# Performance work log

Hardware: AMD Instinct MI355X
Metric: run time of the kernel (lower is better)

The kernel has to match this reference:

```python
import jax, jax.numpy as jnp
import numpy as np

B, T, H, A, V, L = 4096, 16, 768, 128, 16, 2

def setup_inputs() -> dict:
    key = jax.random.key(0)
    ks = jax.random.split(key, 8)
    s = 0.02
    return {
        "last_hidden": jax.random.normal(ks[0], (B, T, H), jnp.float32),
        "attention_mask": jnp.ones((B, T), jnp.int64),
        "variety_ids": jax.random.randint(ks[1], (B,), 0, V),
        "Wd": jax.random.normal(ks[2], (V, H, A), jnp.float32) * s,  # per-variety down-proj
        "bd": jnp.zeros((V, A), jnp.float32),
        "Wu": jax.random.normal(ks[3], (V, A, H), jnp.float32) * s,  # per-variety up-proj
        "bu": jnp.zeros((V, H), jnp.float32),
        "Wc": jax.random.normal(ks[4], (L, H), jnp.float32) * s,     # classifier
        "bc": jnp.zeros((L,), jnp.float32),
    }

def reference(last_hidden, attention_mask, variety_ids, Wd, bd, Wu, bu, Wc, bc):
    x = last_hidden[:, 0, :]                                   # (B,H) CLS token
    # Dense grouped adapter: run all V bottleneck adapters, then select per example.
    h = jax.nn.gelu(jnp.einsum('bh,vha->bva', x, Wd) + bd[None])   # (B,V,A)
    u = jnp.einsum('bva,vah->bvh', h, Wu) + bu[None]               # (B,V,H)
    sel = u[jnp.arange(x.shape[0]), variety_ids]                   # (B,H) routed output
    adapted = x + sel                                              # residual bottleneck adapter
    # dropout is identity at p=0.0 / eval
    return adapted @ Wc.T + bc                                     # (B,L) logits
```

## Files before the change

### kernel.cpp

```cpp
#include <hip/hip_runtime.h>
#include <hip/hip_bf16.h>

#define BB 4096
#define TT 16
#define HH 768
#define AA 128
#define VV 16
#define LL 2
#define NCHUNK 6
#define MT 64

typedef __attribute__((ext_vector_type(8))) short short8v;
typedef __attribute__((ext_vector_type(4))) float float4v;

#define WS_OFFS 0
#define WS_ROWS 64
#define WS_WUC  4160
#define WS_BUC  8256
#define WS_WDP  8448

__device__ __forceinline__ unsigned short f2bf(float f) {
    __hip_bfloat16 h = __float2bfloat16(f);
    return *reinterpret_cast<unsigned short*>(&h);
}

__device__ __forceinline__ float gelu_tanh(float z) {
    float y = 0.7978845608028654f * (z + 0.044715f * z * z * z);
    y = fminf(fmaxf(y, -15.f), 15.f);
    float e = __expf(2.f * y);
    float th = (e - 1.f) / (e + 1.f);
    return 0.5f * z * (1.f + th);
}

__global__ __launch_bounds__(256) void k_prep(
    const int*   __restrict__ variety_ids,
    const float* __restrict__ Wd,
    const float* __restrict__ Wu,
    const float* __restrict__ bu,
    const float* __restrict__ Wc,
    int* __restrict__ ws_i)
{
    __shared__ __align__(16) unsigned short Wds[128 * 136];
    __shared__ float sp0[256], sp1[256];
    __shared__ int hist[VV], hoff[VV + 1], hcur[VV];

    const int t = threadIdx.x;
    const int bid = blockIdx.x;
    unsigned short* wdp = (unsigned short*)(ws_i + WS_WDP);
    float* Wuc = (float*)(ws_i + WS_WUC);
    float* buc = (float*)(ws_i + WS_BUC);

    if (bid < 96) {
        const int v = bid / NCHUNK, kc = bid % NCHUNK;
        const float* wd = Wd + (size_t)v * HH * AA;
        const int ks0 = kc * 128;
        #pragma unroll
        for (int s = 0; s < 16; ++s) {
            int idx = t + s * 256;
            int hl  = idx >> 5;
            int a4  = idx & 31;
            float4 wv = *(const float4*)(wd + (size_t)(ks0 + hl) * AA + a4 * 4);
            Wds[(a4 * 4 + 0) * 136 + hl] = f2bf(wv.x);
            Wds[(a4 * 4 + 1) * 136 + hl] = f2bf(wv.y);
            Wds[(a4 * 4 + 2) * 136 + hl] = f2bf(wv.z);
            Wds[(a4 * 4 + 3) * 136 + hl] = f2bf(wv.w);
        }
        __syncthreads();
        unsigned short* dst = wdp + (size_t)(v * NCHUNK + kc) * AA * 128;
        #pragma unroll
        for (int s = 0; s < 8; ++s) {
            int G = t + s * 256;
            int a = G >> 4, g = G & 15;
            uint4 w = *(const uint4*)&Wds[a * 136 + g * 8];
            *(uint4*)&dst[a * 128 + g * 8] = w;
        }
    } else if (bid < 128) {
        const int v  = (bid - 96) >> 1;
        const int ah = (bid - 96) & 1;
        const int a  = ah * 64 + (t >> 2);
        const int q  = t & 3;
        const float* wu = Wu + (size_t)v * AA * HH + (size_t)a * HH;
        float s0 = 0.f, s1 = 0.f;
        #pragma unroll 4
        for (int h = q * 192; h < q * 192 + 192; h += 4) {
            float4 w  = *(const float4*)&wu[h];
            float4 c0 = *(const float4*)&Wc[h];
            float4 c1 = *(const float4*)&Wc[HH + h];
            s0 += w.x * c0.x + w.y * c0.y + w.z * c0.z + w.w * c0.w;
            s1 += w.x * c1.x + w.y * c1.y + w.z * c1.z + w.w * c1.w;
        }
        sp0[t] = s0; sp1[t] = s1;
        __syncthreads();
        if (t < 64) {
            float r0 = sp0[t * 4] + sp0[t * 4 + 1] + sp0[t * 4 + 2] + sp0[t * 4 + 3];
            float r1 = sp1[t * 4] + sp1[t * 4 + 1] + sp1[t * 4 + 2] + sp1[t * 4 + 3];
            int aa = ah * 64 + t;
            Wuc[(v * AA + aa) * LL + 0] = r0;
            Wuc[(v * AA + aa) * LL + 1] = r1;
        }
    } else if (bid == 128) {
        const int pair = t >> 3, seg = t & 7;
        const int v = pair >> 1, l = pair & 1;
        float s = 0.f;
        const float* bv = bu + (size_t)v * HH;
        for (int h = seg * 96; h < seg * 96 + 96; ++h) s += bv[h] * Wc[l * HH + h];
        sp0[t] = s;
        __syncthreads();
        if (t < 32) {
            float r = 0.f;
            #pragma unroll
            for (int i = 0; i < 8; ++i) r += sp0[t * 8 + i];
            buc[t] = r;
        }
    } else {
        if (t < VV) hist[t] = 0;
        __syncthreads();
        for (int b = t; b < BB; b += 256) atomicAdd(&hist[variety_ids[b]], 1);
        __syncthreads();
        if (t == 0) {
            int s = 0;
            for (int i = 0; i < VV; ++i) { hoff[i] = s; s += hist[i]; }
            hoff[VV] = s;
            for (int i = 0; i <= VV; ++i) ws_i[WS_OFFS + i] = hoff[i];
        }
        __syncthreads();
        if (t < VV) hcur[t] = hoff[t];
        __syncthreads();
        for (int b = t; b < BB; b += 256) {
            int v = variety_ids[b];
            int p = atomicAdd(&hcur[v], 1);
            ws_i[WS_ROWS + p] = b;
        }
    }
}

__global__ __launch_bounds__(256) void k_main(
    const float* __restrict__ last_hidden,
    const int*   __restrict__ ws_i,
    const float* __restrict__ bd,
    const float* __restrict__ Wc,
    const float* __restrict__ bc,
    float* __restrict__ out)
{
    __shared__ __align__(16) unsigned short Xs[MT * 136];
    __shared__ __align__(16) unsigned short Wds[128 * 136];
    __shared__ __align__(16) unsigned short WcB[16 * 136];
    __shared__ int srows[MT];
    __shared__ float xc[MT * LL];

    const int* offs = ws_i + WS_OFFS;
    const int* rows = ws_i + WS_ROWS;
    const float* Wuc = (const float*)(ws_i + WS_WUC);
    const float* buc = (const float*)(ws_i + WS_BUC);
    const unsigned short* wdp = (const unsigned short*)(ws_i + WS_WDP);
    const int t = threadIdx.x;

    const int rt = blockIdx.x;
    int v = -1, tloc = 0, cnt = 0, obase = 0, acc_t = 0;
    for (int vv = 0; vv < VV; ++vv) {
        int c  = offs[vv + 1] - offs[vv];
        int nt = (c + MT - 1) / MT;
        if (rt < acc_t + nt) {
            v = vv; tloc = rt - acc_t;
            cnt = c - tloc * MT; if (cnt > MT) cnt = MT;
            obase = offs[vv];
            break;
        }
        acc_t += nt;
    }
    if (v < 0) return;

    if (t < MT) {
        int rr = t < cnt ? t : cnt - 1;
        srows[t] = rows[obase + tloc * MT + rr];
    }

    const int lane = t & 63;
    const int wv_  = t >> 6;
    const int wr = (wv_ >> 1) * 32;
    const int wc = (wv_ & 1) * 64;
    const int m = lane & 15, quad = lane >> 4;

    float4v acc[2][4];
    float4v accx[2];
    #pragma unroll
    for (int i = 0; i < 2; ++i) {
        accx[i] = (float4v){0.f, 0.f, 0.f, 0.f};
        #pragma unroll
        for (int j = 0; j < 4; ++j)
            acc[i][j] = (float4v){0.f, 0.f, 0.f, 0.f};
    }

    for (int kc = 0; kc < NCHUNK; ++kc) {
        const int ks0 = kc * 128;
        __syncthreads();
        #pragma unroll
        for (int s = 0; s < 8; ++s) {
            int idx = t + s * 256;
            int r   = idx >> 5;
            int k4  = idx & 31;
            const float* xr = last_hidden + (size_t)srows[r] * TT * HH + ks0 + k4 * 4;
            float4 xv = *(const float4*)xr;
            unsigned int p0 = (unsigned)f2bf(xv.x) | ((unsigned)f2bf(xv.y) << 16);
            unsigned int p1 = (unsigned)f2bf(xv.z) | ((unsigned)f2bf(xv.w) << 16);
            *(uint2*)&Xs[r * 136 + k4 * 4] = make_uint2(p0, p1);
        }
        {
            const unsigned short* wb = wdp + (size_t)(v * NCHUNK + kc) * AA * 128;
            #pragma unroll
            for (int s = 0; s < 8; ++s) {
                int G = t + s * 256;
                int a = G >> 4, g = G & 15;
                uint4 w = *(const uint4*)&wb[a * 128 + g * 8];
                *(uint4*)&Wds[a * 136 + g * 8] = w;
            }
        }
        {
            int c = t >> 4, g = t & 15;
            uint4 w = make_uint4(0u, 0u, 0u, 0u);
            if (c < LL) {
                const float* wcr = Wc + (size_t)c * HH + ks0 + g * 8;
                float4 w0 = *(const float4*)wcr;
                float4 w1 = *(const float4*)(wcr + 4);
                w.x = (unsigned)f2bf(w0.x) | ((unsigned)f2bf(w0.y) << 16);
                w.y = (unsigned)f2bf(w0.z) | ((unsigned)f2bf(w0.w) << 16);
                w.z = (unsigned)f2bf(w1.x) | ((unsigned)f2bf(w1.y) << 16);
                w.w = (unsigned)f2bf(w1.z) | ((unsigned)f2bf(w1.w) << 16);
            }
            *(uint4*)&WcB[c * 136 + g * 8] = w;
        }
        __syncthreads();

        #pragma unroll
        for (int k0 = 0; k0 < 128; k0 += 32) {
            short8v af[2], bf[4];
            #pragma unroll
            for (int i = 0; i < 2; ++i)
                af[i] = *(const short8v*)&Xs[(wr + i * 16 + m) * 136 + k0 + quad * 8];
            #pragma unroll
            for (int j = 0; j < 4; ++j)
                bf[j] = *(const short8v*)&Wds[(wc + j * 16 + m) * 136 + k0 + quad * 8];
            #pragma unroll
            for (int i = 0; i < 2; ++i)
                #pragma unroll
                for (int j = 0; j < 4; ++j)
                    acc[i][j] = __builtin_amdgcn_mfma_f32_16x16x32_bf16(af[i], bf[j], acc[i][j], 0, 0, 0);
            if (wc == 0) {
                short8v cf = *(const short8v*)&WcB[m * 136 + k0 + quad * 8];
                #pragma unroll
                for (int i = 0; i < 2; ++i)
                    accx[i] = __builtin_amdgcn_mfma_f32_16x16x32_bf16(af[i], cf, accx[i], 0, 0, 0);
            }
        }
    }

    __syncthreads();
    float* p_part = (float*)Wds;

    {
        const int wch = wc >> 6;
        float bdv[4], w0v[4], w1v[4];
        #pragma unroll
        for (int j = 0; j < 4; ++j) {
            int a = wc + j * 16 + m;
            bdv[j] = bd[v * AA + a];
            w0v[j] = Wuc[(v * AA + a) * LL + 0];
            w1v[j] = Wuc[(v * AA + a) * LL + 1];
        }
        #pragma unroll
        for (int i = 0; i < 2; ++i) {
            #pragma unroll
            for (int reg = 0; reg < 4; ++reg) {
                int row = wr + i * 16 + quad * 4 + reg;
                float p0 = 0.f, p1 = 0.f;
                #pragma unroll
                for (int j = 0; j < 4; ++j) {
                    float h = gelu_tanh(acc[i][j][reg] + bdv[j]);
                    p0 += h * w0v[j];
                    p1 += h * w1v[j];
                }
                p_part[(row * LL + 0) * 32 + wch * 16 + m] = p0;
                p_part[(row * LL + 1) * 32 + wch * 16 + m] = p1;
            }
        }
        if (wc == 0 && m < LL) {
            #pragma unroll
            for (int i = 0; i < 2; ++i)
                #pragma unroll
                for (int reg = 0; reg < 4; ++reg) {
                    int row = wr + i * 16 + quad * 4 + reg;
                    xc[row * LL + m] = accx[i][reg];
                }
        }
    }
    __syncthreads();

    if (t < MT * LL) {
        int row = t >> 1, l = t & 1;
        if (row < cnt) {
            float s = 0.f;
            #pragma unroll
            for (int k = 0; k < 32; ++k) s += p_part[(row * LL + l) * 32 + k];
            int gr = srows[row];
            out[(size_t)gr * LL + l] = s + xc[row * LL + l] + buc[v * LL + l] + bc[l];
        }
    }
}

extern "C" void kernel_launch(void* const* d_in, const int* in_sizes, int n_in,
                              void* d_out, int out_size, void* d_ws, size_t ws_size,
                              hipStream_t stream) {
    const float* last_hidden = (const float*)d_in[0];
    const int*   variety_ids = (const int*)d_in[2];
    const float* Wd = (const float*)d_in[3];
    const float* bd = (const float*)d_in[4];
    const float* Wu = (const float*)d_in[5];
    const float* bu = (const float*)d_in[6];
    const float* Wc = (const float*)d_in[7];
    const float* bc = (const float*)d_in[8];
    float* out = (float*)d_out;

    int* ws_i = (int*)d_ws;

    k_prep<<<130, 256, 0, stream>>>(variety_ids, Wd, Wu, bu, Wc, ws_i);
    k_main<<<79, 256, 0, stream>>>(last_hidden, ws_i, bd, Wc, bc, out);
}
```

Baseline: 279.8 us.

## Shrink row tile to 16 and widen prep grid for more parallel blocks

Reduces the per-block row tile from 64 to 16 rows so the main kernel launches about 271 blocks instead of 79, filling more of the GPU's compute units. The MFMA warp layout is rebuilt so each of the four waves covers 32 adapter columns for all 16 rows, and the partial-sum reduction now spans 64 entries. The Wu·Wc precompute in the prep kernel is split across 128 blocks instead of 32, each with shorter dot products. In exchange, each Wd chunk is reloaded by four times as many blocks, which adds L2 traffic and per-block overhead.

```diff
diff --git a/kernel.cpp b/kernel.cpp
--- a/kernel.cpp
+++ b/kernel.cpp
@@ -8,7 +8,7 @@
 #define VV 16
 #define LL 2
 #define NCHUNK 6
-#define MT 64
+#define MT 16
 
 typedef __attribute__((ext_vector_type(8))) short short8v;
 typedef __attribute__((ext_vector_type(4))) float float4v;
@@ -74,31 +74,34 @@
             uint4 w = *(const uint4*)&Wds[a * 136 + g * 8];
             *(uint4*)&dst[a * 128 + g * 8] = w;
         }
-    } else if (bid < 128) {
-        const int v  = (bid - 96) >> 1;
-        const int ah = (bid - 96) & 1;
-        const int a  = ah * 64 + (t >> 2);
-        const int q  = t & 3;
+    } else if (bid < 224) {
+        const int v = (bid - 96) >> 3;
+        const int g = (bid - 96) & 7;
+        const int a_loc = t >> 4;
+        const int q     = t & 15;
+        const int a = g * 16 + a_loc;
         const float* wu = Wu + (size_t)v * AA * HH + (size_t)a * HH;
         float s0 = 0.f, s1 = 0.f;
         #pragma unroll 4
-        for (int h = q * 192; h < q * 192 + 192; h += 4) {
+        for (int h = q * 48; h < q * 48 + 48; h += 4) {
             float4 w  = *(const float4*)&wu[h];
             float4 c0 = *(const float4*)&Wc[h];
             float4 c1 = *(const float4*)&Wc[HH + h];
             s0 += w.x * c0.x + w.y * c0.y + w.z * c0.z + w.w * c0.w;
             s1 += w.x * c1.x + w.y * c1.y + w.z * c1.z + w.w * c1.w;
         }
-        sp0[t] = s0; sp1[t] = s1;
-        __syncthreads();
-        if (t < 64) {
-            float r0 = sp0[t * 4] + sp0[t * 4 + 1] + sp0[t * 4 + 2] + sp0[t * 4 + 3];
-            float r1 = sp1[t * 4] + sp1[t * 4 + 1] + sp1[t * 4 + 2] + sp1[t * 4 + 3];
-            int aa = ah * 64 + t;
+        sp0[a_loc * 16 + q] = s0;
+        sp1[a_loc * 16 + q] = s1;
+        __syncthreads();
+        if (t < 16) {
+            float r0 = 0.f, r1 = 0.f;
+            #pragma unroll
+            for (int i = 0; i < 16; ++i) { r0 += sp0[t * 16 + i]; r1 += sp1[t * 16 + i]; }
+            int aa = g * 16 + t;
             Wuc[(v * AA + aa) * LL + 0] = r0;
             Wuc[(v * AA + aa) * LL + 1] = r1;
         }
-    } else if (bid == 128) {
+    } else if (bid == 224) {
         const int pair = t >> 3, seg = t & 7;
         const int v = pair >> 1, l = pair & 1;
         float s = 0.f;
@@ -177,25 +180,20 @@
 
     const int lane = t & 63;
     const int wv_  = t >> 6;
-    const int wr = (wv_ >> 1) * 32;
-    const int wc = (wv_ & 1) * 64;
+    const int ac0  = wv_ * 32;
     const int m = lane & 15, quad = lane >> 4;
 
-    float4v acc[2][4];
-    float4v accx[2];
-    #pragma unroll
-    for (int i = 0; i < 2; ++i) {
-        accx[i] = (float4v){0.f, 0.f, 0.f, 0.f};
-        #pragma unroll
-        for (int j = 0; j < 4; ++j)
-            acc[i][j] = (float4v){0.f, 0.f, 0.f, 0.f};
-    }
+    float4v acc[2];
+    float4v accx;
+    acc[0] = (float4v){0.f, 0.f, 0.f, 0.f};
+    acc[1] = (float4v){0.f, 0.f, 0.f, 0.f};
+    accx   = (float4v){0.f, 0.f, 0.f, 0.f};
 
     for (int kc = 0; kc < NCHUNK; ++kc) {
         const int ks0 = kc * 128;
         __syncthreads();
         #pragma unroll
-        for (int s = 0; s < 8; ++s) {
+        for (int s = 0; s < 2; ++s) {
             int idx = t + s * 256;
             int r   = idx >> 5;
             int k4  = idx & 31;
@@ -233,23 +231,14 @@
 
         #pragma unroll
         for (int k0 = 0; k0 < 128; k0 += 32) {
-            short8v af[2], bf[4];
-            #pragma unroll
-            for (int i = 0; i < 2; ++i)
-                af[i] = *(const short8v*)&Xs[(wr + i * 16 + m) * 136 + k0 + quad * 8];
-            #pragma unroll
-            for (int j = 0; j < 4; ++j)
-                bf[j] = *(const short8v*)&Wds[(wc + j * 16 + m) * 136 + k0 + quad * 8];
-            #pragma unroll
-            for (int i = 0; i < 2; ++i)
-                #pragma unroll
-                for (int j = 0; j < 4; ++j)
-                    acc[i][j] = __builtin_amdgcn_mfma_f32_16x16x32_bf16(af[i], bf[j], acc[i][j], 0, 0, 0);
-            if (wc == 0) {
+            short8v af = *(const short8v*)&Xs[m * 136 + k0 + quad * 8];
+            short8v bf0 = *(const short8v*)&Wds[(ac0 + m) * 136 + k0 + quad * 8];
+            short8v bf1 = *(const short8v*)&Wds[(ac0 + 16 + m) * 136 + k0 + quad * 8];
+            acc[0] = __builtin_amdgcn_mfma_f32_16x16x32_bf16(af, bf0, acc[0], 0, 0, 0);
+            acc[1] = __builtin_amdgcn_mfma_f32_16x16x32_bf16(af, bf1, acc[1], 0, 0, 0);
+            if (wv_ == 0) {
                 short8v cf = *(const short8v*)&WcB[m * 136 + k0 + quad * 8];
-                #pragma unroll
-                for (int i = 0; i < 2; ++i)
-                    accx[i] = __builtin_amdgcn_mfma_f32_16x16x32_bf16(af[i], cf, accx[i], 0, 0, 0);
+                accx = __builtin_amdgcn_mfma_f32_16x16x32_bf16(af, cf, accx, 0, 0, 0);
             }
         }
     }
@@ -258,39 +247,33 @@
     float* p_part = (float*)Wds;
 
     {
-        const int wch = wc >> 6;
-        float bdv[4], w0v[4], w1v[4];
-        #pragma unroll
-        for (int j = 0; j < 4; ++j) {
-            int a = wc + j * 16 + m;
+        float bdv[2], w0v[2], w1v[2];
+        #pragma unroll
+        for (int j = 0; j < 2; ++j) {
+            int a = ac0 + j * 16 + m;
             bdv[j] = bd[v * AA + a];
             w0v[j] = Wuc[(v * AA + a) * LL + 0];
             w1v[j] = Wuc[(v * AA + a) * LL + 1];
         }
         #pragma unroll
-        for (int i = 0; i < 2; ++i) {
+        for (int reg = 0; reg < 4; ++reg) {
+            int row = quad * 4 + reg;
+            float p0 = 0.f, p1 = 0.f;
+            #pragma unroll
+            for (int j = 0; j < 2; ++j) {
+                float h = gelu_tanh(acc[j][reg] + bdv[j]);
+                p0 += h * w0v[j];
+                p1 += h * w1v[j];
+            }
+            p_part[(row * LL + 0) * 64 + wv_ * 16 + m] = p0;
+            p_part[(row * LL + 1) * 64 + wv_ * 16 + m] = p1;
+        }
+        if (wv_ == 0 && m < LL) {
             #pragma unroll
             for (int reg = 0; reg < 4; ++reg) {
-                int row = wr + i * 16 + quad * 4 + reg;
-                float p0 = 0.f, p1 = 0.f;
-                #pragma unroll
-                for (int j = 0; j < 4; ++j) {
-                    float h = gelu_tanh(acc[i][j][reg] + bdv[j]);
-                    p0 += h * w0v[j];
-                    p1 += h * w1v[j];
-                }
-                p_part[(row * LL + 0) * 32 + wch * 16 + m] = p0;
-                p_part[(row * LL + 1) * 32 + wch * 16 + m] = p1;
-            }
-        }
-        if (wc == 0 && m < LL) {
-            #pragma unroll
-            for (int i = 0; i < 2; ++i)
-                #pragma unroll
-                for (int reg = 0; reg < 4; ++reg) {
-                    int row = wr + i * 16 + quad * 4 + reg;
-                    xc[row * LL + m] = accx[i][reg];
-                }
+                int row = quad * 4 + reg;
+                xc[row * LL + m] = accx[reg];
+            }
         }
     }
     __syncthreads();
@@ -300,7 +283,7 @@
         if (row < cnt) {
             float s = 0.f;
             #pragma unroll
-            for (int k = 0; k < 32; ++k) s += p_part[(row * LL + l) * 32 + k];
+            for (int k = 0; k < 64; ++k) s += p_part[(row * LL + l) * 64 + k];
             int gr = srows[row];
             out[(size_t)gr * LL + l] = s + xc[row * LL + l] + buc[v * LL + l] + bc[l];
         }
@@ -322,6 +305,6 @@
 
     int* ws_i = (int*)d_ws;
 
-    k_prep<<<130, 256, 0, stream>>>(variety_ids, Wd, Wu, bu, Wc, ws_i);
-    k_main<<<79, 256, 0, stream>>>(last_hidden, ws_i, bd, Wc, bc, out);
-}
+    k_prep<<<226, 256, 0, stream>>>(variety_ids, Wd, Wu, bu, Wc, ws_i);
+    k_main<<<271, 256, 0, stream>>>(last_hidden, ws_i, bd, Wc, bc, out);
+}
```

New measurement: 271.2 us. -3.1%, faster.
